# Kernel optimization log

Hardware: AMD Instinct MI355X
Metric: run time of the kernel (lower is better)

## Reference

```python
import jax, jax.numpy as jnp
import numpy as np

N, DH, DK, FF = 2048, 256, 64, 32


def setup_inputs() -> dict:
    key = jax.random.key(0)
    ks = jax.random.split(key, 12)
    s = lambda d: 1.0 / np.sqrt(d).astype(np.float32)
    return {
        "x": jax.random.normal(ks[0], (1, N, DH), dtype=jnp.float32),
        "adj": (jax.random.uniform(ks[1], (N, N)) < 0.05).astype(jnp.float32),
        "dense": jax.random.uniform(ks[2], (N, N), dtype=jnp.float32),
        "Wq": jax.random.normal(ks[3], (DH, DK)) * s(DH),
        "bq": jnp.zeros((DK,), jnp.float32),
        "Wk": jax.random.normal(ks[4], (DH, DK)) * s(DH),
        "bk": jnp.zeros((DK,), jnp.float32),
        "Wv": jax.random.normal(ks[5], (DH, DH)) * s(DH),
        "bv": jnp.zeros((DH,), jnp.float32),
        "W1": jax.random.normal(ks[6], (3, FF)) * s(3),
        "b1": jnp.zeros((FF,), jnp.float32),
        "W2": jax.random.normal(ks[7], (FF, FF)) * s(FF),
        "b2": jnp.zeros((FF,), jnp.float32),
        "W3": jax.random.normal(ks[8], (FF, 1)) * s(FF),
        "b3": jnp.zeros((1,), jnp.float32),
    }


def reference(x, adj, dense, Wq, bq, Wk, bk, Wv, bv, W1, b1, W2, b2, W3, b3):
    # x: (1, n, dh). Original repeats x to (n, n, dh); here we exploit that
    # q[i, j] = Q(x_j), k[i, j] = K(x_i), v[i, j] = V(x_j) so no n^2*dh tensor
    # is materialized, while the math is identical.
    x0 = x[0]                      # (n, dh)
    q = x0 @ Wq + bq               # (n, dk), Q(x_j)
    k = x0 @ Wk + bk               # (n, dk), K(x_i)
    v = x0 @ Wv + bv               # (n, dh), V(x_j)
    # out[i, j] = <Q(x_j), K(x_i)>
    scores = k @ q.T               # (n, n)
    feats = jnp.stack((scores, adj, dense), axis=2)      # (n, n, 3)
    h = jax.nn.relu(feats @ W1 + b1)                     # (n, n, FF)
    h = jax.nn.relu(h @ W2 + b2)                         # (n, n, FF)
    focus = jax.nn.softmax((h @ W3 + b3)[..., 0], axis=1)  # (n, n)
    # feature[i] = sum_j focus[i, j] * V(x_j)
    feature = focus @ v            # (n, dh)
    return feature[None]           # (1, n, dh)
```

## Files before the change

kernel.cpp:

```cpp
#include <hip/hip_runtime.h>
#include <math.h>


#define NN  2048
#define DHH 256
#define DKK 64

typedef float    f32x4 __attribute__((ext_vector_type(4)));
typedef _Float16 f16x8 __attribute__((ext_vector_type(8)));
typedef _Float16 f16x4 __attribute__((ext_vector_type(4)));
typedef _Float16 f16x2 __attribute__((ext_vector_type(2)));

__device__ __forceinline__ float dpp_sum16(float x) {
    int v;
    v = __builtin_amdgcn_update_dpp(0, __builtin_bit_cast(int, x), 0x118, 0xf, 0xf, true);
    x += __builtin_bit_cast(float, v);
    v = __builtin_amdgcn_update_dpp(0, __builtin_bit_cast(int, x), 0x114, 0xf, 0xf, true);
    x += __builtin_bit_cast(float, v);
    v = __builtin_amdgcn_update_dpp(0, __builtin_bit_cast(int, x), 0x112, 0xf, 0xf, true);
    x += __builtin_bit_cast(float, v);
    v = __builtin_amdgcn_update_dpp(0, __builtin_bit_cast(int, x), 0x111, 0xf, 0xf, true);
    x += __builtin_bit_cast(float, v);
    return x;
}

__global__ __launch_bounds__(256) void k_qkv(
    const float* __restrict__ x,
    const float* __restrict__ Wq, const float* __restrict__ bq,
    const float* __restrict__ Wk, const float* __restrict__ bk,
    const float* __restrict__ Wv, const float* __restrict__ bv,
    _Float16* __restrict__ q16, _Float16* __restrict__ k16,
    _Float16* __restrict__ vT)
{
    __shared__ float As[32][64];
    __shared__ float Bs[32][64];
    __shared__ _Float16 Ts[64 * 72];

    const int t  = threadIdx.x;
    const int m0 = blockIdx.x * 64;
    const int yb = blockIdx.y;

    const float* W; const float* bias; int wld; int cw0;
    if (yb == 0)      { W = Wq; bias = bq; wld = 64;  cw0 = 0; }
    else if (yb == 1) { W = Wk; bias = bk; wld = 64;  cw0 = 0; }
    else              { W = Wv; bias = bv; wld = 256; cw0 = (yb - 2) * 64; }

    const int tx = t & 15, ty = t >> 4;
    float acc[4][4] = {};

    for (int k0 = 0; k0 < DHH; k0 += 32) {
        {
            const int rr = t >> 3;
            const int cc = (t & 7) * 4;
            float4 a0 = *(const float4*)(x + (size_t)(m0 + rr)      * DHH + k0 + cc);
            float4 a1 = *(const float4*)(x + (size_t)(m0 + rr + 32) * DHH + k0 + cc);
            As[cc+0][rr]    = a0.x; As[cc+1][rr]    = a0.y; As[cc+2][rr]    = a0.z; As[cc+3][rr]    = a0.w;
            As[cc+0][rr+32] = a1.x; As[cc+1][rr+32] = a1.y; As[cc+2][rr+32] = a1.z; As[cc+3][rr+32] = a1.w;
        }
        {
            const int bk_ = t >> 4;
            const int bc  = (t & 15) * 4;
            *(float4*)&Bs[bk_][bc]      = *(const float4*)(W + (size_t)(k0 + bk_)      * wld + cw0 + bc);
            *(float4*)&Bs[bk_ + 16][bc] = *(const float4*)(W + (size_t)(k0 + bk_ + 16) * wld + cw0 + bc);
        }
        __syncthreads();
        #pragma unroll
        for (int kk = 0; kk < 32; ++kk) {
            float4 a = *(const float4*)&As[kk][ty * 4];
            float4 b = *(const float4*)&Bs[kk][tx * 4];
            float av[4] = {a.x, a.y, a.z, a.w};
            float bw[4] = {b.x, b.y, b.z, b.w};
            #pragma unroll
            for (int ii = 0; ii < 4; ++ii)
                #pragma unroll
                for (int jj = 0; jj < 4; ++jj)
                    acc[ii][jj] = fmaf(av[ii], bw[jj], acc[ii][jj]);
        }
        __syncthreads();
    }

    float4 b4 = *(const float4*)&bias[cw0 + tx * 4];
    float bc4[4] = {b4.x, b4.y, b4.z, b4.w};

    if (yb < 2) {
        _Float16* outp = (yb == 0) ? q16 : k16;
        #pragma unroll
        for (int ii = 0; ii < 4; ++ii) {
            f16x4 hv;
            #pragma unroll
            for (int jj = 0; jj < 4; ++jj) hv[jj] = (_Float16)(acc[ii][jj] + bc4[jj]);
            *(f16x4*)&outp[(size_t)(m0 + ty * 4 + ii) * 64 + tx * 4] = hv;
        }
    } else {
        #pragma unroll
        for (int jj = 0; jj < 4; ++jj) {
            f16x4 hv;
            #pragma unroll
            for (int ii = 0; ii < 4; ++ii) hv[ii] = (_Float16)(acc[ii][jj] + bc4[jj]);
            *(f16x4*)&Ts[(tx * 4 + jj) * 72 + ty * 4] = hv;
        }
        __syncthreads();
        {
            const int c = t >> 2, seg = t & 3;
            f16x8 r0 = *(const f16x8*)&Ts[c * 72 + seg * 16];
            f16x8 r1 = *(const f16x8*)&Ts[c * 72 + seg * 16 + 8];
            *(f16x8*)&vT[(size_t)(cw0 + c) * NN + m0 + seg * 16]     = r0;
            *(f16x8*)&vT[(size_t)(cw0 + c) * NN + m0 + seg * 16 + 8] = r1;
        }
    }
}

__global__ __launch_bounds__(256) void k_scores(
    const _Float16* __restrict__ q16, const _Float16* __restrict__ k16,
    _Float16* __restrict__ schi, _Float16* __restrict__ sclo)
{
    const int t    = threadIdx.x;
    const int lane = t & 63;
    const int w    = t >> 6;
    const int col  = lane & 15;
    const int q    = lane >> 4;

    const int i0 = blockIdx.y * 128 + (w >> 1) * 64;
    const int j0 = blockIdx.x * 128 + (w & 1) * 64;

    f32x4 acc[4][4] = {};

    #pragma unroll
    for (int ks = 0; ks < 2; ++ks) {
        f16x8 a[4], b[4];
        #pragma unroll
        for (int f = 0; f < 4; ++f) {
            a[f] = *(const f16x8*)&k16[(size_t)(i0 + f * 16 + col) * 64 + ks * 32 + q * 8];
            b[f] = *(const f16x8*)&q16[(size_t)(j0 + f * 16 + col) * 64 + ks * 32 + q * 8];
        }
        #pragma unroll
        for (int fm = 0; fm < 4; ++fm)
            #pragma unroll
            for (int fn = 0; fn < 4; ++fn)
                acc[fm][fn] = __builtin_amdgcn_mfma_f32_16x16x32_f16(a[fm], b[fn], acc[fm][fn], 0, 0, 0);
    }

    #pragma unroll
    for (int fm = 0; fm < 4; ++fm)
        #pragma unroll
        for (int fn = 0; fn < 4; ++fn)
            #pragma unroll
            for (int r = 0; r < 4; ++r) {
                const size_t idx = (size_t)(i0 + fm * 16 + q * 4 + r) * NN + j0 + fn * 16 + col;
                const float val = acc[fm][fn][r];
                const _Float16 h = (_Float16)val;
                schi[idx] = h;
                sclo[idx] = (_Float16)(val - (float)h);
            }
}

__global__ __launch_bounds__(256) void k_mlp(
    const _Float16* __restrict__ schi, const _Float16* __restrict__ sclo,
    const float* __restrict__ adj, const float* __restrict__ dense,
    const float* __restrict__ W1, const float* __restrict__ b1,
    const float* __restrict__ W2, const float* __restrict__ b2,
    const float* __restrict__ W3, const float* __restrict__ b3,
    _Float16* __restrict__ fhi)
{
    __shared__ _Float16 fA[4][64 * 8];
    __shared__ _Float16 hs[4][64 * 40];
    __shared__ _Float16 zsh[8];
    __shared__ float    lsg[NN];
    __shared__ float    red[8];

    const int t    = threadIdx.x;
    const int lane = t & 63;
    const int w    = t >> 6;
    const int col  = lane & 15;
    const int q    = lane >> 4;
    const int i    = blockIdx.x;

    if (t < 8) zsh[t] = (_Float16)0;
    __syncthreads();

    f16x8 w1f0 = {}, w1f1 = {};
    if (q == 0) {
        const int ne = 2 * col, no = 2 * col + 1;
        const float w0e = W1[0*32 + ne], w0o = W1[0*32 + no];
        const _Float16 w0eh = (_Float16)w0e, w0oh = (_Float16)w0o;
        w1f0[0] = w0eh; w1f0[1] = w0eh;
        w1f0[2] = (_Float16)W1[1*32 + ne];
        w1f0[3] = (_Float16)W1[2*32 + ne];
        w1f0[4] = (_Float16)(w0e - (float)w0eh);
        w1f1[0] = w0oh; w1f1[1] = w0oh;
        w1f1[2] = (_Float16)W1[1*32 + no];
        w1f1[3] = (_Float16)W1[2*32 + no];
        w1f1[4] = (_Float16)(w0o - (float)w0oh);
    }
    f16x8 w2f0, w2f1;
    #pragma unroll
    for (int j = 0; j < 8; ++j) {
        w2f0[j] = (_Float16)W2[(q * 8 + j) * 32 + col];
        w2f1[j] = (_Float16)W2[(q * 8 + j) * 32 + col + 16];
    }
    const float b1e = b1[2 * col], b1o = b1[2 * col + 1];
    const float b2a = b2[col],     b2b = b2[col + 16];
    const float w3a = W3[col],     w3b = W3[col + 16];
    const float b3v = b3[0];

    const _Float16* shrow = schi + (size_t)i * NN;
    const _Float16* slrow = sclo + (size_t)i * NN;
    const float*    arow  = adj   + (size_t)i * NN;
    const float*    drow  = dense + (size_t)i * NN;

    const f32x4 zero4 = {0.f, 0.f, 0.f, 0.f};

    for (int c = 0; c < 8; ++c) {
        const int base = w * 512 + c * 64;
        const int jj   = base + lane;

        {
            const _Float16 sh = shrow[jj];
            const _Float16 sl = slrow[jj];
            f16x8 fv = {sh, sl, (_Float16)arow[jj], (_Float16)drow[jj],
                        sh, (_Float16)0, (_Float16)0, (_Float16)0};
            *(f16x8*)&fA[w][lane * 8] = fv;
        }
        asm volatile("s_waitcnt lgkmcnt(0)" ::: "memory");

        #pragma unroll
        for (int st = 0; st < 4; ++st) {
            const _Float16* ap = (q == 0) ? &fA[w][(st * 16 + col) * 8] : zsh;
            f16x8 af = *(const f16x8*)ap;
            f32x4 hp0 = __builtin_amdgcn_mfma_f32_16x16x32_f16(af, w1f0, zero4, 0, 0, 0);
            f32x4 hp1 = __builtin_amdgcn_mfma_f32_16x16x32_f16(af, w1f1, zero4, 0, 0, 0);
            #pragma unroll
            for (int r = 0; r < 4; ++r) {
                f16x2 pk;
                pk[0] = (_Float16)fmaxf(hp0[r] + b1e, 0.f);
                pk[1] = (_Float16)fmaxf(hp1[r] + b1o, 0.f);
                *(f16x2*)&hs[w][(st * 16 + q * 4 + r) * 40 + col * 2] = pk;
            }
        }
        asm volatile("s_waitcnt lgkmcnt(0)" ::: "memory");

        #pragma unroll
        for (int st = 0; st < 4; ++st) {
            f16x8 a2 = *(const f16x8*)&hs[w][(st * 16 + col) * 40 + q * 8];
            f32x4 acc0 = __builtin_amdgcn_mfma_f32_16x16x32_f16(a2, w2f0, zero4, 0, 0, 0);
            f32x4 acc1 = __builtin_amdgcn_mfma_f32_16x16x32_f16(a2, w2f1, zero4, 0, 0, 0);
            float p[4];
            #pragma unroll
            for (int r = 0; r < 4; ++r) {
                p[r] = fmaxf(acc0[r] + b2a, 0.f) * w3a + fmaxf(acc1[r] + b2b, 0.f) * w3b;
                p[r] = dpp_sum16(p[r]);
            }
            if (col == 15) {
                float4 lgv = {p[0] + b3v, p[1] + b3v, p[2] + b3v, p[3] + b3v};
                *(float4*)&lsg[base + st * 16 + q * 4] = lgv;
            }
        }
        asm volatile("s_waitcnt lgkmcnt(0)" ::: "memory");
    }
    __syncthreads();

    float lv[8], lmax = -1e30f;
    #pragma unroll
    for (int u = 0; u < 8; ++u) { lv[u] = lsg[t + u * 256]; lmax = fmaxf(lmax, lv[u]); }
    #pragma unroll
    for (int off = 32; off > 0; off >>= 1)
        lmax = fmaxf(lmax, __shfl_xor(lmax, off, 64));
    if (lane == 0) red[w] = lmax;
    __syncthreads();
    const float rmax = fmaxf(fmaxf(red[0], red[1]), fmaxf(red[2], red[3]));

    float wgt[8], lsum = 0.f;
    #pragma unroll
    for (int u = 0; u < 8; ++u) { wgt[u] = __expf(lv[u] - rmax); lsum += wgt[u]; }
    #pragma unroll
    for (int off = 32; off > 0; off >>= 1)
        lsum += __shfl_xor(lsum, off, 64);
    if (lane == 0) red[4 + w] = lsum;
    __syncthreads();
    const float inv = 1.f / (red[4] + red[5] + red[6] + red[7]);

    _Float16* hrow = fhi + (size_t)i * NN;
    #pragma unroll
    for (int u = 0; u < 8; ++u)
        hrow[t + u * 256] = (_Float16)(wgt[u] * inv);
}

__global__ __launch_bounds__(256) void k_feat(
    const _Float16* __restrict__ fhi, const _Float16* __restrict__ vT,
    float* __restrict__ out)
{
    const int t    = threadIdx.x;
    const int lane = t & 63;
    const int w    = t >> 6;
    const int col  = lane & 15;
    const int q    = lane >> 4;

    const int m0 = blockIdx.y * 16;
    const int n0 = blockIdx.x * 128 + w * 32;

    f32x4 acc[2] = {};

    const size_t arow  = (size_t)(m0 + col) * NN;
    const size_t brow0 = (size_t)(n0 + col) * NN;
    const size_t brow1 = (size_t)(n0 + 16 + col) * NN;

    for (int k0 = 0; k0 < NN; k0 += 32) {
        const int ko = k0 + q * 8;
        f16x8 a  = *(const f16x8*)&fhi[arow + ko];
        f16x8 b0 = *(const f16x8*)&vT[brow0 + ko];
        f16x8 b1 = *(const f16x8*)&vT[brow1 + ko];
        acc[0] = __builtin_amdgcn_mfma_f32_16x16x32_f16(a, b0, acc[0], 0, 0, 0);
        acc[1] = __builtin_amdgcn_mfma_f32_16x16x32_f16(a, b1, acc[1], 0, 0, 0);
    }

    #pragma unroll
    for (int fn = 0; fn < 2; ++fn)
        #pragma unroll
        for (int r = 0; r < 4; ++r)
            out[(size_t)(m0 + q * 4 + r) * DHH + n0 + fn * 16 + col] = acc[fn][r];
}

extern "C" void kernel_launch(void* const* d_in, const int* in_sizes, int n_in,
                              void* d_out, int out_size, void* d_ws, size_t ws_size,
                              hipStream_t stream) {
    const float* x     = (const float*)d_in[0];
    const float* adj   = (const float*)d_in[1];
    const float* dense = (const float*)d_in[2];
    const float* Wq    = (const float*)d_in[3];
    const float* bq    = (const float*)d_in[4];
    const float* Wk    = (const float*)d_in[5];
    const float* bk    = (const float*)d_in[6];
    const float* Wv    = (const float*)d_in[7];
    const float* bv    = (const float*)d_in[8];
    const float* W1    = (const float*)d_in[9];
    const float* b1    = (const float*)d_in[10];
    const float* W2    = (const float*)d_in[11];
    const float* b2    = (const float*)d_in[12];
    const float* W3    = (const float*)d_in[13];
    const float* b3    = (const float*)d_in[14];
    float* out = (float*)d_out;

    char* wsb = (char*)d_ws;
    _Float16* q16  = (_Float16*)(wsb);
    _Float16* k16  = (_Float16*)(wsb + 262144);
    _Float16* vT   = (_Float16*)(wsb + 524288);
    _Float16* schi = (_Float16*)(wsb + 1572864);
    _Float16* sclo = (_Float16*)(wsb + 9961472);

    hipLaunchKernelGGL(k_qkv,    dim3(32, 6),  dim3(256), 0, stream,
                       x, Wq, bq, Wk, bk, Wv, bv, q16, k16, vT);
    hipLaunchKernelGGL(k_scores, dim3(16, 16), dim3(256), 0, stream, q16, k16, schi, sclo);
    hipLaunchKernelGGL(k_mlp,    dim3(2048),   dim3(256), 0, stream,
                       schi, sclo, adj, dense, W1, b1, W2, b2, W3, b3, schi);
    hipLaunchKernelGGL(k_feat,   dim3(2, 128), dim3(256), 0, stream,
                       schi, vT, out);
}
```

Baseline: 195.0 us.

## Fuse MLP layers per subtile, fold biases into MFMA, split-K feature GEMM

In the MLP kernel, layer 1 and layer 2 now run per 16-row subtile, which shrinks the shared hidden buffer and drops one sync pass. Biases are preloaded into the MFMA accumulators, and layer 2 is transposed so the W3 dot product becomes a per-lane FMA plus two cross-lane shuffles, replacing the DPP reduction. The b3 bias is dropped, which is valid because softmax is shift-invariant. The feature GEMM now splits K across the four waves and reduces partials through shared memory, running four times as many blocks to raise parallelism at the cost of an extra sync and reduction.

```diff
diff --git a/kernel.cpp b/kernel.cpp
--- a/kernel.cpp
+++ b/kernel.cpp
@@ -10,19 +10,6 @@
 typedef _Float16 f16x8 __attribute__((ext_vector_type(8)));
 typedef _Float16 f16x4 __attribute__((ext_vector_type(4)));
 typedef _Float16 f16x2 __attribute__((ext_vector_type(2)));
-
-__device__ __forceinline__ float dpp_sum16(float x) {
-    int v;
-    v = __builtin_amdgcn_update_dpp(0, __builtin_bit_cast(int, x), 0x118, 0xf, 0xf, true);
-    x += __builtin_bit_cast(float, v);
-    v = __builtin_amdgcn_update_dpp(0, __builtin_bit_cast(int, x), 0x114, 0xf, 0xf, true);
-    x += __builtin_bit_cast(float, v);
-    v = __builtin_amdgcn_update_dpp(0, __builtin_bit_cast(int, x), 0x112, 0xf, 0xf, true);
-    x += __builtin_bit_cast(float, v);
-    v = __builtin_amdgcn_update_dpp(0, __builtin_bit_cast(int, x), 0x111, 0xf, 0xf, true);
-    x += __builtin_bit_cast(float, v);
-    return x;
-}
 
 __global__ __launch_bounds__(256) void k_qkv(
     const float* __restrict__ x,
@@ -159,11 +146,11 @@
     const float* __restrict__ adj, const float* __restrict__ dense,
     const float* __restrict__ W1, const float* __restrict__ b1,
     const float* __restrict__ W2, const float* __restrict__ b2,
-    const float* __restrict__ W3, const float* __restrict__ b3,
+    const float* __restrict__ W3,
     _Float16* __restrict__ fhi)
 {
     __shared__ _Float16 fA[4][64 * 8];
-    __shared__ _Float16 hs[4][64 * 40];
+    __shared__ _Float16 hs[4][16 * 40];
     __shared__ _Float16 zsh[8];
     __shared__ float    lsg[NN];
     __shared__ float    red[8];
@@ -199,26 +186,29 @@
         w2f1[j] = (_Float16)W2[(q * 8 + j) * 32 + col + 16];
     }
     const float b1e = b1[2 * col], b1o = b1[2 * col + 1];
-    const float b2a = b2[col],     b2b = b2[col + 16];
-    const float w3a = W3[col],     w3b = W3[col + 16];
-    const float b3v = b3[0];
+    const f32x4 c1e = {b1e, b1e, b1e, b1e};
+    const f32x4 c1o = {b1o, b1o, b1o, b1o};
+    f32x4 c2a, c2b, w3v, w3v2;
+    #pragma unroll
+    for (int r = 0; r < 4; ++r) {
+        c2a[r]  = b2[q * 4 + r];
+        c2b[r]  = b2[16 + q * 4 + r];
+        w3v[r]  = W3[q * 4 + r];
+        w3v2[r] = W3[16 + q * 4 + r];
+    }
 
     const _Float16* shrow = schi + (size_t)i * NN;
     const _Float16* slrow = sclo + (size_t)i * NN;
     const float*    arow  = adj   + (size_t)i * NN;
     const float*    drow  = dense + (size_t)i * NN;
 
-    const f32x4 zero4 = {0.f, 0.f, 0.f, 0.f};
-
     for (int c = 0; c < 8; ++c) {
         const int base = w * 512 + c * 64;
         const int jj   = base + lane;
 
         {
-            const _Float16 sh = shrow[jj];
-            const _Float16 sl = slrow[jj];
-            f16x8 fv = {sh, sl, (_Float16)arow[jj], (_Float16)drow[jj],
-                        sh, (_Float16)0, (_Float16)0, (_Float16)0};
+            f16x8 fv = {shrow[jj], slrow[jj], (_Float16)arow[jj], (_Float16)drow[jj],
+                        shrow[jj], (_Float16)0, (_Float16)0, (_Float16)0};
             *(f16x8*)&fA[w][lane * 8] = fv;
         }
         asm volatile("s_waitcnt lgkmcnt(0)" ::: "memory");
@@ -227,35 +217,30 @@
         for (int st = 0; st < 4; ++st) {
             const _Float16* ap = (q == 0) ? &fA[w][(st * 16 + col) * 8] : zsh;
             f16x8 af = *(const f16x8*)ap;
-            f32x4 hp0 = __builtin_amdgcn_mfma_f32_16x16x32_f16(af, w1f0, zero4, 0, 0, 0);
-            f32x4 hp1 = __builtin_amdgcn_mfma_f32_16x16x32_f16(af, w1f1, zero4, 0, 0, 0);
+            f32x4 hp0 = __builtin_amdgcn_mfma_f32_16x16x32_f16(af, w1f0, c1e, 0, 0, 0);
+            f32x4 hp1 = __builtin_amdgcn_mfma_f32_16x16x32_f16(af, w1f1, c1o, 0, 0, 0);
             #pragma unroll
             for (int r = 0; r < 4; ++r) {
-                f16x2 pk;
-                pk[0] = (_Float16)fmaxf(hp0[r] + b1e, 0.f);
-                pk[1] = (_Float16)fmaxf(hp1[r] + b1o, 0.f);
-                *(f16x2*)&hs[w][(st * 16 + q * 4 + r) * 40 + col * 2] = pk;
+                f16x2 pk = __builtin_bit_cast(f16x2,
+                    __builtin_amdgcn_cvt_pkrtz(fmaxf(hp0[r], 0.f), fmaxf(hp1[r], 0.f)));
+                *(f16x2*)&hs[w][(q * 4 + r) * 40 + col * 2] = pk;
             }
-        }
-        asm volatile("s_waitcnt lgkmcnt(0)" ::: "memory");
-
-        #pragma unroll
-        for (int st = 0; st < 4; ++st) {
-            f16x8 a2 = *(const f16x8*)&hs[w][(st * 16 + col) * 40 + q * 8];
-            f32x4 acc0 = __builtin_amdgcn_mfma_f32_16x16x32_f16(a2, w2f0, zero4, 0, 0, 0);
-            f32x4 acc1 = __builtin_amdgcn_mfma_f32_16x16x32_f16(a2, w2f1, zero4, 0, 0, 0);
-            float p[4];
+            asm volatile("s_waitcnt lgkmcnt(0)" ::: "memory");
+
+            f16x8 a2 = *(const f16x8*)&hs[w][col * 40 + q * 8];
+            f32x4 acc0 = __builtin_amdgcn_mfma_f32_16x16x32_f16(w2f0, a2, c2a, 0, 0, 0);
+            f32x4 acc1 = __builtin_amdgcn_mfma_f32_16x16x32_f16(w2f1, a2, c2b, 0, 0, 0);
+            float p = 0.f;
             #pragma unroll
             for (int r = 0; r < 4; ++r) {
-                p[r] = fmaxf(acc0[r] + b2a, 0.f) * w3a + fmaxf(acc1[r] + b2b, 0.f) * w3b;
-                p[r] = dpp_sum16(p[r]);
+                p = fmaf(fmaxf(acc0[r], 0.f), w3v[r],  p);
+                p = fmaf(fmaxf(acc1[r], 0.f), w3v2[r], p);
             }
-            if (col == 15) {
-                float4 lgv = {p[0] + b3v, p[1] + b3v, p[2] + b3v, p[3] + b3v};
-                *(float4*)&lsg[base + st * 16 + q * 4] = lgv;
-            }
-        }
-        asm volatile("s_waitcnt lgkmcnt(0)" ::: "memory");
+            p += __shfl_xor(p, 16, 64);
+            p += __shfl_xor(p, 32, 64);
+            if (q == st) lsg[base + st * 16 + col] = p;
+            asm volatile("s_waitcnt lgkmcnt(0)" ::: "memory");
+        }
     }
     __syncthreads();
 
@@ -289,6 +274,8 @@
     const _Float16* __restrict__ fhi, const _Float16* __restrict__ vT,
     float* __restrict__ out)
 {
+    __shared__ float rbuf[3][64][8];
+
     const int t    = threadIdx.x;
     const int lane = t & 63;
     const int w    = t >> 6;
@@ -296,28 +283,45 @@
     const int q    = lane >> 4;
 
     const int m0 = blockIdx.y * 16;
-    const int n0 = blockIdx.x * 128 + w * 32;
-
-    f32x4 acc[2] = {};
+    const int n0 = blockIdx.x * 32;
+
+    f32x4 acc0 = {}, acc1 = {};
 
     const size_t arow  = (size_t)(m0 + col) * NN;
     const size_t brow0 = (size_t)(n0 + col) * NN;
     const size_t brow1 = (size_t)(n0 + 16 + col) * NN;
-
-    for (int k0 = 0; k0 < NN; k0 += 32) {
-        const int ko = k0 + q * 8;
+    const int kb = w * 512 + q * 8;
+
+    #pragma unroll 4
+    for (int k0 = 0; k0 < 512; k0 += 32) {
+        const int ko = kb + k0;
         f16x8 a  = *(const f16x8*)&fhi[arow + ko];
         f16x8 b0 = *(const f16x8*)&vT[brow0 + ko];
         f16x8 b1 = *(const f16x8*)&vT[brow1 + ko];
-        acc[0] = __builtin_amdgcn_mfma_f32_16x16x32_f16(a, b0, acc[0], 0, 0, 0);
-        acc[1] = __builtin_amdgcn_mfma_f32_16x16x32_f16(a, b1, acc[1], 0, 0, 0);
-    }
-
-    #pragma unroll
-    for (int fn = 0; fn < 2; ++fn)
-        #pragma unroll
-        for (int r = 0; r < 4; ++r)
-            out[(size_t)(m0 + q * 4 + r) * DHH + n0 + fn * 16 + col] = acc[fn][r];
+        acc0 = __builtin_amdgcn_mfma_f32_16x16x32_f16(a, b0, acc0, 0, 0, 0);
+        acc1 = __builtin_amdgcn_mfma_f32_16x16x32_f16(a, b1, acc1, 0, 0, 0);
+    }
+
+    if (w != 0) {
+        *(float4*)&rbuf[w - 1][lane][0] = *(float4*)&acc0;
+        *(float4*)&rbuf[w - 1][lane][4] = *(float4*)&acc1;
+    }
+    __syncthreads();
+
+    if (w == 0) {
+        #pragma unroll
+        for (int j = 0; j < 3; ++j) {
+            float4 p0 = *(const float4*)&rbuf[j][lane][0];
+            float4 p1 = *(const float4*)&rbuf[j][lane][4];
+            acc0[0] += p0.x; acc0[1] += p0.y; acc0[2] += p0.z; acc0[3] += p0.w;
+            acc1[0] += p1.x; acc1[1] += p1.y; acc1[2] += p1.z; acc1[3] += p1.w;
+        }
+        #pragma unroll
+        for (int r = 0; r < 4; ++r) {
+            out[(size_t)(m0 + q * 4 + r) * DHH + n0 + col]      = acc0[r];
+            out[(size_t)(m0 + q * 4 + r) * DHH + n0 + 16 + col] = acc1[r];
+        }
+    }
 }
 
 extern "C" void kernel_launch(void* const* d_in, const int* in_sizes, int n_in,
@@ -337,7 +341,6 @@
     const float* W2    = (const float*)d_in[11];
     const float* b2    = (const float*)d_in[12];
     const float* W3    = (const float*)d_in[13];
-    const float* b3    = (const float*)d_in[14];
     float* out = (float*)d_out;
 
     char* wsb = (char*)d_ws;
@@ -351,7 +354,7 @@
                        x, Wq, bq, Wk, bk, Wv, bv, q16, k16, vT);
     hipLaunchKernelGGL(k_scores, dim3(16, 16), dim3(256), 0, stream, q16, k16, schi, sclo);
     hipLaunchKernelGGL(k_mlp,    dim3(2048),   dim3(256), 0, stream,
-                       schi, sclo, adj, dense, W1, b1, W2, b2, W3, b3, schi);
-    hipLaunchKernelGGL(k_feat,   dim3(2, 128), dim3(256), 0, stream,
+                       schi, sclo, adj, dense, W1, b1, W2, b2, W3, schi);
+    hipLaunchKernelGGL(k_feat,   dim3(8, 128), dim3(256), 0, stream,
                        schi, vT, out);
 }
```

After: 183.8 us. -5.7%, faster.
